# Optimization experiments

Measured on AMD Instinct MI355X. Metric: run time of the kernel, lower is better.

The kernel has to match this reference:

```python
import jax, jax.numpy as jnp
import numpy as np
from jax import lax

SPARSITY = 0.5  # args.sparsity: fraction of weights KEPT


def get_subnet(scores, k):
    """GetSubnet.forward: sort |scores|, zero lowest (1-k) fraction, one elsewhere."""
    sa = jnp.abs(scores)
    n = sa.size
    j = int((1.0 - k) * n)  # static: number of entries zeroed
    idx = jnp.argsort(sa.ravel())  # ascending, matches torch .sort()
    mask = jnp.zeros((n,), dtype=sa.dtype).at[idx[j:]].set(1.0)
    return mask.reshape(scores.shape)


def masked_conv(x, w, s, b, stride):
    m = get_subnet(s, SPARSITY)
    y = lax.conv_general_dilated(
        x, w * m, window_strides=(stride, stride), padding=((1, 1), (1, 1)),
        dimension_numbers=('NCHW', 'OIHW', 'NCHW'))
    return y + b[None, :, None, None]


def setup_inputs() -> dict:
    key = jax.random.key(0)
    ks = jax.random.split(key, 16)
    def rn(k, shape, scale):
        return jax.random.normal(k, shape, dtype=jnp.float32) * scale
    return {
        'x':   rn(ks[0], (64, 3, 64, 64), 1.0),
        'w1':  rn(ks[1], (128, 3, 3, 3), 0.2),   's1': rn(ks[2], (128, 3, 3, 3), 1.0),   'b1': rn(ks[3], (128,), 0.01),
        'w2':  rn(ks[4], (256, 128, 3, 3), 0.05), 's2': rn(ks[5], (256, 128, 3, 3), 1.0), 'b2': rn(ks[6], (256,), 0.01),
        'w3':  rn(ks[7], (512, 256, 3, 3), 0.03), 's3': rn(ks[8], (512, 256, 3, 3), 1.0), 'b3': rn(ks[9], (512,), 0.01),
        'fw1': rn(ks[10], (1024, 512), 0.05),     'fs1': rn(ks[11], (1024, 512), 1.0),    'fb1': rn(ks[12], (1024,), 0.01),
        'fw2': rn(ks[13], (10, 1024), 0.05),      'fs2': rn(ks[14], (10, 1024), 1.0),     'fb2': rn(ks[15], (10,), 0.01),
    }


def reference(x, w1, s1, b1, w2, s2, b2, w3, s3, b3, fw1, fs1, fb1, fw2, fs2, fb2):
    h = jax.nn.relu(masked_conv(x, w1, s1, b1, stride=1))   # [64,128,64,64]
    h = jax.nn.relu(masked_conv(h, w2, s2, b2, stride=2))   # [64,256,32,32]
    h = jax.nn.relu(masked_conv(h, w3, s3, b3, stride=2))   # [64,512,16,16]
    h = h.mean(axis=(2, 3))                                 # [64,512] global avg pool
    m1 = get_subnet(fs1, SPARSITY)
    h = jax.nn.relu(h @ (fw1 * m1).T + fb1)                 # [64,1024]
    m2 = get_subnet(fs2, SPARSITY)
    return h @ (fw2 * m2).T + fb2                           # [64,10]
```

## Files before the change

### kernel.cpp

```cpp
#include <hip/hip_runtime.h>
#include <stdint.h>


typedef __attribute__((ext_vector_type(8))) short short8;
typedef __attribute__((ext_vector_type(4))) short short4v;
typedef __attribute__((ext_vector_type(4))) float floatx4;

__device__ __forceinline__ unsigned short f2bf(float f) {
    unsigned u = __float_as_uint(f);
    u += 0x7fffu + ((u >> 16) & 1u);
    return (unsigned short)(u >> 16);
}

constexpr unsigned CUM0 = 3456u;
constexpr unsigned CUM1 = 298368u;
constexpr unsigned CUM2 = 1478016u;
constexpr unsigned CUM3 = 2002304u;
constexpr unsigned STOT = 2012544u;
constexpr int NBH = 512;

__device__ __forceinline__ int find_tensor(unsigned idx, unsigned& li) {
    if (idx < CUM0) { li = idx;        return 0; }
    if (idx < CUM1) { li = idx - CUM0; return 1; }
    if (idx < CUM2) { li = idx - CUM1; return 2; }
    if (idx < CUM3) { li = idx - CUM2; return 3; }
    li = idx - CUM3; return 4;
}

__global__ __launch_bounds__(256) void hist11(const float* __restrict__ s0,
                                              const float* __restrict__ s1,
                                              const float* __restrict__ s2,
                                              const float* __restrict__ s3,
                                              const float* __restrict__ s4,
                                              const unsigned* __restrict__ P,
                                              unsigned* __restrict__ ghist, int pass) {
    __shared__ unsigned lh[10240];
    const int tid = threadIdx.x;
    const int NB = (pass == 2) ? 512 : 2048;
    for (int i = tid; i < NB * 5; i += 256) lh[i] = 0;
    __syncthreads();

    unsigned pref[5];
    #pragma unroll
    for (int t = 0; t < 5; t++) pref[t] = pass ? P[t] : 0u;
    const int fsh = (pass == 1) ? 20 : 9;

    for (unsigned idx = blockIdx.x * 256u + tid; idx < STOT; idx += NBH * 256u) {
        unsigned li; int t = find_tensor(idx, li);
        const float* sp = t == 0 ? s0 : t == 1 ? s1 : t == 2 ? s2 : t == 3 ? s3 : s4;
        unsigned key = __float_as_uint(sp[li]) & 0x7fffffffu;
        bool ok = (pass == 0) || ((key >> fsh) == pref[t]);
        if (ok) {
            unsigned bin = (pass == 0) ? (key >> 20)
                         : (pass == 1) ? ((key >> 9) & 2047u)
                                       : (key & 511u);
            atomicAdd(&lh[(unsigned)t * NB + bin], 1u);
        }
    }
    __syncthreads();
    const int goff = (pass == 0) ? 0 : (pass == 1) ? 10240 : 20480;
    for (int i = tid; i < NB * 5; i += 256) {
        unsigned v = lh[i];
        if (v) atomicAdd(&ghist[goff + i], v);
    }
}

__global__ __launch_bounds__(256) void find11(const unsigned* __restrict__ ghist,
                                              unsigned* __restrict__ P,
                                              unsigned* __restrict__ targ, int pass) {
    const int t = blockIdx.x;
    const int tid = threadIdx.x;
    const int NB = (pass == 2) ? 512 : 2048;
    const int goff = (pass == 0) ? 0 : (pass == 1) ? 10240 : 20480;
    const int seg = NB / 256;
    __shared__ unsigned bins[2048];
    __shared__ unsigned part[256];
    for (int i = tid; i < NB; i += 256) bins[i] = ghist[goff + t * NB + i];
    __syncthreads();
    unsigned s = 0;
    for (int j = 0; j < seg; j++) s += bins[tid * seg + j];
    part[tid] = s;
    __syncthreads();
    if (tid == 0) {
        unsigned n = t == 0 ? 3456u : t == 1 ? 294912u : t == 2 ? 1179648u
                   : t == 3 ? 524288u : 10240u;
        unsigned target = (pass == 0) ? (n >> 1) : targ[t];
        unsigned cum = 0; int q = 0;
        for (; q < 256; q++) { unsigned c = part[q]; if (cum + c > target) break; cum += c; }
        int b = q * seg;
        for (;; b++) { unsigned c = bins[b]; if (cum + c > target) break; cum += c; }
        targ[t] = target - cum;
        if (pass == 0)      P[t] = (unsigned)b;
        else if (pass == 1) P[t] = (P[t] << 11) | (unsigned)b;
        else                P[t] = (P[t] << 9) | (unsigned)b;
    }
}

__global__ void mask_reorder(const float* __restrict__ w0, const float* __restrict__ w1,
                             const float* __restrict__ w2, const float* __restrict__ w3,
                             const float* __restrict__ w4,
                             const float* __restrict__ s0, const float* __restrict__ s1,
                             const float* __restrict__ s2, const float* __restrict__ s3,
                             const float* __restrict__ s4,
                             const unsigned* __restrict__ T,
                             float* __restrict__ wm1,
                             unsigned short* __restrict__ A2,
                             unsigned short* __restrict__ A3,
                             float* __restrict__ fwm1, float* __restrict__ fwm2,
                             float* __restrict__ pooled) {
    unsigned idx = blockIdx.x * 256u + threadIdx.x;
    if (idx >= STOT) return;
    if (idx < 32768u) pooled[idx] = 0.f;
    unsigned li; int t = find_tensor(idx, li);
    const float* sp = t == 0 ? s0 : t == 1 ? s1 : t == 2 ? s2 : t == 3 ? s3 : s4;
    const float* wp = t == 0 ? w0 : t == 1 ? w1 : t == 2 ? w2 : t == 3 ? w3 : w4;
    unsigned key = __float_as_uint(sp[li]) & 0x7fffffffu;
    float val = (key >= T[t]) ? wp[li] : 0.f;
    if (t == 0) {
        wm1[li] = val;
    } else if (t == 1) {
        unsigned k = li / 1152u, r = li - k * 1152u;
        unsigned c = r / 9u, e = r - c * 9u;
        A2[((size_t)e * 256u + k) * 128u + c] = f2bf(val);
    } else if (t == 2) {
        unsigned k = li / 2304u, r = li - k * 2304u;
        unsigned c = r / 9u, e = r - c * 9u;
        A3[((size_t)e * 512u + k) * 256u + c] = f2bf(val);
    } else if (t == 3) {
        fwm1[li] = val;
    } else {
        fwm2[li] = val;
    }
}

template <int C, int H, int W, int K, int TX, int TY, int KT>
__global__ __launch_bounds__(TX* TY) void conv_direct(const float* __restrict__ in,
                                                      const float* __restrict__ wm,
                                                      const float* __restrict__ bias,
                                                      unsigned short* __restrict__ out) {
    constexpr int TILW = TX * 2, TILH = TY * 2;
    constexpr int ITW = TILW + 2, ITH = TILH + 2;
    constexpr int NTHREADS = TX * TY;
    constexpr int NLOAD = (ITH * ITW + NTHREADS - 1) / NTHREADS;
    constexpr int KG = K / KT;

    __shared__ float sIn[ITH * ITW];
    __shared__ float sW[9 * KT];

    const int tid = threadIdx.x;
    const int tx = tid % TX, ty = tid / TX;
    const int kg = blockIdx.z % KG, n = blockIdx.z / KG;
    const int ox0 = blockIdx.x * TILW, oy0 = blockIdx.y * TILH;
    const int ix0 = ox0 - 1, iy0 = oy0 - 1;

    const float* inN = in + (size_t)n * C * H * W;
    const float* wkg = wm + (size_t)kg * KT * C * 9;

    int goff[NLOAD];
    #pragma unroll
    for (int i = 0; i < NLOAD; i++) {
        int idx = tid + i * NTHREADS;
        if (idx < ITH * ITW) {
            int r = idx / ITW, col = idx % ITW;
            int gy = iy0 + r, gx = ix0 + col;
            goff[i] = (gy >= 0 && gy < H && gx >= 0 && gx < W) ? (gy * W + gx) : -1;
        } else goff[i] = -2;
    }

    float acc[2][2][KT];
    #pragma unroll
    for (int py = 0; py < 2; py++)
        #pragma unroll
        for (int px = 0; px < 2; px++)
            #pragma unroll
            for (int j = 0; j < KT; j++) acc[py][px][j] = 0.f;

    for (int c = 0; c < C; c++) {
        const float* inC = inN + (size_t)c * H * W;
        #pragma unroll
        for (int i = 0; i < NLOAD; i++) {
            int g = goff[i];
            if (g >= -1) sIn[tid + i * NTHREADS] = (g >= 0) ? inC[g] : 0.f;
        }
        for (int i = tid; i < 9 * KT; i += NTHREADS) {
            int e = i / KT, j = i % KT;
            sW[i] = wkg[j * C * 9 + c * 9 + e];
        }
        __syncthreads();

        float vin[4][4];
        const float* base = &sIn[(ty * 2) * ITW + tx * 2];
        #pragma unroll
        for (int r = 0; r < 4; r++)
            #pragma unroll
            for (int cc = 0; cc < 4; cc++) vin[r][cc] = base[r * ITW + cc];

        #pragma unroll
        for (int e = 0; e < 9; e++) {
            const int dy = e / 3, dx = e % 3;
            #pragma unroll
            for (int j = 0; j < KT; j++) {
                float wv = sW[e * KT + j];
                #pragma unroll
                for (int py = 0; py < 2; py++)
                    #pragma unroll
                    for (int px = 0; px < 2; px++)
                        acc[py][px][j] = fmaf(vin[py + dy][px + dx], wv, acc[py][px][j]);
            }
        }
        __syncthreads();
    }

    float bj[KT];
    #pragma unroll
    for (int j = 0; j < KT; j++) bj[j] = bias[kg * KT + j];
    #pragma unroll
    for (int py = 0; py < 2; py++)
        #pragma unroll
        for (int px = 0; px < 2; px++) {
            int oy = oy0 + ty * 2 + py, ox = ox0 + tx * 2 + px;
            short8 v;
            #pragma unroll
            for (int j = 0; j < KT; j++) {
                float t = acc[py][px][j] + bj[j];
                v[j] = (short)f2bf(t > 0.f ? t : 0.f);
            }
            *(short8*)(out + ((size_t)(n * H + oy) * W + ox) * K + kg * KT) = v;
        }
}

template <int C, int H, int W, int KOUT, int NPIX, bool POOL, bool SWAPYZ>
__global__ __launch_bounds__(256, 4) void conv_mfma(const unsigned short* __restrict__ in,
                                                    const unsigned short* __restrict__ A,
                                                    const float* __restrict__ bias,
                                                    void* __restrict__ outv) {
    constexpr int OH = H / 2, OW = W / 2;
    constexpr int PR = NPIX / OW;
    constexpr int FN = NPIX / 16;
    constexpr int RH = 2 * PR + 1;
    constexpr int IW = W + 1;
    constexpr int NC = C / 32;
    constexpr int PSTR = 40;
    constexpr int NSLOT = RH * IW * 4;
    constexpr int SLMAX = (NSLOT + 255) / 256;

    __shared__ unsigned short sIn[RH * IW * PSTR];

    const int tid = threadIdx.x;
    const int lane = tid & 63;
    const int wv = tid >> 6;
    const int l15 = lane & 15;
    const int quad = lane >> 4;
    const int pt = blockIdx.x;
    const int kb = SWAPYZ ? blockIdx.z : blockIdx.y;
    const int n  = SWAPYZ ? blockIdx.y : blockIdx.z;
    const int k0 = kb * 128;
    const int oy0 = pt * PR;
    const int g0y = 2 * oy0 - 1;
    const int mw = wv * 32;

    int goff[SLMAX], slds[SLMAX];
    #pragma unroll
    for (int i = 0; i < SLMAX; i++) {
        int s = tid + i * 256;
        if (s < NSLOT) {
            int q = s & 3, pix = s >> 2;
            int ix = pix % IW, iy = pix / IW;
            int gy = g0y + iy, gx = ix - 1;
            slds[i] = pix * PSTR + q * 8;
            goff[i] = (gy >= 0 && gy < H && gx >= 0) ? ((gy * W + gx) * C + q * 8) : -1;
        } else { goff[i] = -2; slds[i] = 0; }
    }

    int pB[FN];
    #pragma unroll
    for (int fn = 0; fn < FN; fn++) {
        int p = fn * 16 + l15;
        int oyl = p / OW, oxl = p % OW;
        pB[fn] = (oyl * 2 * IW + oxl * 2) * PSTR + quad * 8;
    }

    const unsigned short* inN = in + (size_t)n * H * W * C;

    floatx4 acc[2][FN];
    #pragma unroll
    for (int fm = 0; fm < 2; fm++)
        #pragma unroll
        for (int fn = 0; fn < FN; fn++) acc[fm][fn] = (floatx4){0.f, 0.f, 0.f, 0.f};

    short8 st[SLMAX];
    #pragma unroll
    for (int i = 0; i < SLMAX; i++) {
        int g = goff[i];
        if (g >= 0) st[i] = *(const short8*)(inN + g);
    }

    for (int cc = 0; cc < NC; cc++) {
        const int cof = cc * 32;
        #pragma unroll
        for (int i = 0; i < SLMAX; i++) {
            int g = goff[i];
            if (g >= 0) {
                *(short8*)&sIn[slds[i]] = st[i];
            } else if (g == -1 && cc == 0) {
                *(short8*)&sIn[slds[i]] = (short8){0, 0, 0, 0, 0, 0, 0, 0};
            }
        }
        __syncthreads();
        if (cc + 1 < NC) {
            const int ncof = cof + 32;
            #pragma unroll
            for (int i = 0; i < SLMAX; i++) {
                int g = goff[i];
                if (g >= 0) st[i] = *(const short8*)(inN + g + ncof);
            }
        }

        const unsigned short* Abase = A + (size_t)(k0 + mw + l15) * C + cof + quad * 8;
        const size_t estr = (size_t)KOUT * C;

        short8 a0 = *(const short8*)(Abase);
        short8 a1 = *(const short8*)(Abase + 16 * C);

        #pragma unroll 1
        for (int e = 0; e < 9; e++) {
            short8 ac0 = a0, ac1 = a1;
            if (e < 8) {
                a0 = *(const short8*)(Abase + (size_t)(e + 1) * estr);
                a1 = *(const short8*)(Abase + (size_t)(e + 1) * estr + 16 * C);
            }
            const int dy = e / 3, dx = e - dy * 3;
            const int boff = (dy * IW + dx) * PSTR;
            short8 bfr[FN];
            #pragma unroll
            for (int fn = 0; fn < FN; fn++)
                bfr[fn] = *(const short8*)&sIn[pB[fn] + boff];
            #pragma unroll
            for (int fn = 0; fn < FN; fn++) {
                acc[0][fn] = __builtin_amdgcn_mfma_f32_16x16x32_bf16(ac0, bfr[fn], acc[0][fn], 0, 0, 0);
                acc[1][fn] = __builtin_amdgcn_mfma_f32_16x16x32_bf16(ac1, bfr[fn], acc[1][fn], 0, 0, 0);
            }
        }
        __syncthreads();
    }

    if (!POOL) {
        unsigned short* out = (unsigned short*)outv;
        #pragma unroll
        for (int fm = 0; fm < 2; fm++) {
            const int k4 = k0 + mw + fm * 16 + quad * 4;
            float b0 = bias[k4], b1 = bias[k4 + 1], b2 = bias[k4 + 2], b3 = bias[k4 + 3];
            #pragma unroll
            for (int fn = 0; fn < FN; fn++) {
                int p = fn * 16 + l15;
                int oy = oy0 + p / OW, ox = p % OW;
                float v0 = acc[fm][fn][0] + b0, v1 = acc[fm][fn][1] + b1;
                float v2 = acc[fm][fn][2] + b2, v3 = acc[fm][fn][3] + b3;
                short4v v;
                v[0] = (short)f2bf(v0 > 0.f ? v0 : 0.f);
                v[1] = (short)f2bf(v1 > 0.f ? v1 : 0.f);
                v[2] = (short)f2bf(v2 > 0.f ? v2 : 0.f);
                v[3] = (short)f2bf(v3 > 0.f ? v3 : 0.f);
                *(short4v*)(out + ((size_t)(n * OH + oy) * OW + ox) * KOUT + k4) = v;
            }
        }
    } else {
        float* out = (float*)outv;
        #pragma unroll
        for (int fm = 0; fm < 2; fm++) {
            #pragma unroll
            for (int reg = 0; reg < 4; reg++) {
                int k = k0 + mw + fm * 16 + quad * 4 + reg;
                float bv = bias[k];
                float s = 0.f;
                #pragma unroll
                for (int fn = 0; fn < FN; fn++) {
                    float v = acc[fm][fn][reg] + bv;
                    s += v > 0.f ? v : 0.f;
                }
                s += __shfl_xor(s, 1); s += __shfl_xor(s, 2);
                s += __shfl_xor(s, 4); s += __shfl_xor(s, 8);
                if (l15 == 0) atomicAdd(&out[n * KOUT + k], s * (1.0f / (OH * OW)));
            }
        }
    }
}

__global__ void fc1_kernel(const float* __restrict__ pooled, const float* __restrict__ w,
                           const float* __restrict__ b, float* __restrict__ out) {
    int t = blockIdx.x * 256 + threadIdx.x;
    int o = t & 1023, n = t >> 10;
    const float4* w4 = (const float4*)(w + (size_t)o * 512);
    const float4* p4 = (const float4*)(pooled + (size_t)n * 512);
    float acc = 0.f;
    for (int i = 0; i < 128; i++) {
        float4 a = p4[i], ww = w4[i];
        acc += a.x * ww.x + a.y * ww.y + a.z * ww.z + a.w * ww.w;
    }
    acc += b[o];
    out[t] = acc > 0.f ? acc : 0.f;
}

__global__ void fc2_kernel(const float* __restrict__ h, const float* __restrict__ w,
                           const float* __restrict__ b, float* __restrict__ out) {
    int n = blockIdx.x, tid = threadIdx.x;
    __shared__ float redw[40];
    const float4* h4 = (const float4*)(h + (size_t)n * 1024);
    float4 a = h4[tid];
    for (int o = 0; o < 10; o++) {
        const float4* w4 = (const float4*)(w + (size_t)o * 1024);
        float4 ww = w4[tid];
        float v = a.x * ww.x + a.y * ww.y + a.z * ww.z + a.w * ww.w;
        for (int off = 32; off > 0; off >>= 1) v += __shfl_down(v, off);
        if ((tid & 63) == 0) redw[o * 4 + (tid >> 6)] = v;
    }
    __syncthreads();
    if (tid < 10) {
        float s = redw[tid * 4] + redw[tid * 4 + 1] + redw[tid * 4 + 2] + redw[tid * 4 + 3] + b[tid];
        out[n * 10 + tid] = s;
    }
}

extern "C" void kernel_launch(void* const* d_in, const int* in_sizes, int n_in,
                              void* d_out, int out_size, void* d_ws, size_t ws_size,
                              hipStream_t stream) {
    const float* x   = (const float*)d_in[0];
    const float* w1  = (const float*)d_in[1];
    const float* s1  = (const float*)d_in[2];
    const float* b1  = (const float*)d_in[3];
    const float* w2  = (const float*)d_in[4];
    const float* s2  = (const float*)d_in[5];
    const float* b2  = (const float*)d_in[6];
    const float* w3  = (const float*)d_in[7];
    const float* s3  = (const float*)d_in[8];
    const float* b3  = (const float*)d_in[9];
    const float* fw1 = (const float*)d_in[10];
    const float* fs1 = (const float*)d_in[11];
    const float* fb1 = (const float*)d_in[12];
    const float* fw2 = (const float*)d_in[13];
    const float* fs2 = (const float*)d_in[14];
    const float* fb2 = (const float*)d_in[15];
    float* out = (float*)d_out;

    char* ws = (char*)d_ws;
    size_t off = 0;
    auto alloc = [&](size_t bytes) -> char* {
        char* p = ws + off;
        off = (off + bytes + 255) & ~(size_t)255;
        return p;
    };
    unsigned* ghist = (unsigned*)alloc(23040ull * 4);
    unsigned* P     = (unsigned*)alloc(64);
    unsigned* targ  = (unsigned*)alloc(64);
    float* wm1  = (float*)alloc(3456ull * 4);
    float* fwm1 = (float*)alloc(524288ull * 4);
    float* fwm2 = (float*)alloc(10240ull * 4);
    unsigned short* A2 = (unsigned short*)alloc(294912ull * 2);
    unsigned short* A3 = (unsigned short*)alloc(1179648ull * 2);
    unsigned short* h1 = (unsigned short*)alloc(33554432ull * 2);
    unsigned short* h2 = (unsigned short*)alloc(16777216ull * 2);
    float* pooled = (float*)alloc(32768ull * 4);
    float* fc1h   = (float*)alloc(65536ull * 4);
    if (off > ws_size) return;

    (void)hipMemsetAsync(ghist, 0, 23040ull * 4, stream);

    for (int pass = 0; pass < 3; pass++) {
        hist11<<<NBH, 256, 0, stream>>>(s1, s2, s3, fs1, fs2, P, ghist, pass);
        find11<<<5, 256, 0, stream>>>(ghist, P, targ, pass);
    }
    int gs = (STOT + 255) / 256;
    mask_reorder<<<gs, 256, 0, stream>>>(w1, w2, w3, fw1, fw2, s1, s2, s3, fs1, fs2, P,
                                         wm1, A2, A3, fwm1, fwm2, pooled);

    conv_direct<3, 64, 64, 128, 16, 16, 8>
        <<<dim3(2, 2, 64 * 16), 256, 0, stream>>>(x, wm1, b1, h1);
    conv_mfma<128, 64, 64, 256, 64, false, false>
        <<<dim3(16, 2, 64), 256, 0, stream>>>(h1, A2, b2, h2);
    conv_mfma<256, 32, 32, 512, 64, true, true>
        <<<dim3(4, 64, 4), 256, 0, stream>>>(h2, A3, b3, pooled);

    fc1_kernel<<<256, 256, 0, stream>>>(pooled, fwm1, fb1, fc1h);
    fc2_kernel<<<64, 256, 0, stream>>>(fc1h, fwm2, fb2, out);
}
```

Before: 424.2 us.

## Unroll tap loop with deeper A/B fragment prefetch, drop cross-chunk register staging

Drops the register-staged prefetch of the next input channel chunk, which overlapped global loads with compute across chunks. Global input is now loaded straight into LDS each chunk. In its place the 9-tap loop is fully unrolled: weight fragments are prefetched two taps ahead and LDS fragments one tap ahead, so MFMAs can overlap loads within a chunk. This trades the cross-chunk overlap for intra-chunk scheduling and raises register pressure, which may cut occupancy.

Measured after the change: 420.0 us. No clear change (-1.0%).

```diff
diff --git a/kernel.cpp b/kernel.cpp
--- a/kernel.cpp
+++ b/kernel.cpp
@@ -288,60 +288,56 @@
         #pragma unroll
         for (int fn = 0; fn < FN; fn++) acc[fm][fn] = (floatx4){0.f, 0.f, 0.f, 0.f};
 
-    short8 st[SLMAX];
-    #pragma unroll
-    for (int i = 0; i < SLMAX; i++) {
-        int g = goff[i];
-        if (g >= 0) st[i] = *(const short8*)(inN + g);
-    }
-
+    #pragma unroll 1
     for (int cc = 0; cc < NC; cc++) {
         const int cof = cc * 32;
+        const unsigned short* Abase = A + (size_t)(k0 + mw + l15) * C + cof + quad * 8;
+        const size_t estr = (size_t)KOUT * C;
+
+        __syncthreads();
+
+        short8 af[9][2];
+        short8 bf[9][FN];
+
+        af[0][0] = *(const short8*)(Abase);
+        af[0][1] = *(const short8*)(Abase + 16 * C);
+        af[1][0] = *(const short8*)(Abase + estr);
+        af[1][1] = *(const short8*)(Abase + estr + 16 * C);
+
         #pragma unroll
         for (int i = 0; i < SLMAX; i++) {
             int g = goff[i];
             if (g >= 0) {
-                *(short8*)&sIn[slds[i]] = st[i];
+                *(short8*)&sIn[slds[i]] = *(const short8*)(inN + g + cof);
             } else if (g == -1 && cc == 0) {
                 *(short8*)&sIn[slds[i]] = (short8){0, 0, 0, 0, 0, 0, 0, 0};
             }
         }
         __syncthreads();
-        if (cc + 1 < NC) {
-            const int ncof = cof + 32;
-            #pragma unroll
-            for (int i = 0; i < SLMAX; i++) {
-                int g = goff[i];
-                if (g >= 0) st[i] = *(const short8*)(inN + g + ncof);
-            }
-        }
-
-        const unsigned short* Abase = A + (size_t)(k0 + mw + l15) * C + cof + quad * 8;
-        const size_t estr = (size_t)KOUT * C;
-
-        short8 a0 = *(const short8*)(Abase);
-        short8 a1 = *(const short8*)(Abase + 16 * C);
-
-        #pragma unroll 1
+
+        #pragma unroll
+        for (int fn = 0; fn < FN; fn++)
+            bf[0][fn] = *(const short8*)&sIn[pB[fn]];
+
+        #pragma unroll
         for (int e = 0; e < 9; e++) {
-            short8 ac0 = a0, ac1 = a1;
-            if (e < 8) {
-                a0 = *(const short8*)(Abase + (size_t)(e + 1) * estr);
-                a1 = *(const short8*)(Abase + (size_t)(e + 1) * estr + 16 * C);
-            }
-            const int dy = e / 3, dx = e - dy * 3;
-            const int boff = (dy * IW + dx) * PSTR;
-            short8 bfr[FN];
-            #pragma unroll
-            for (int fn = 0; fn < FN; fn++)
-                bfr[fn] = *(const short8*)&sIn[pB[fn] + boff];
+            if (e + 2 < 9) {
+                af[e + 2][0] = *(const short8*)(Abase + (size_t)(e + 2) * estr);
+                af[e + 2][1] = *(const short8*)(Abase + (size_t)(e + 2) * estr + 16 * C);
+            }
+            if (e + 1 < 9) {
+                const int dy1 = (e + 1) / 3, dx1 = (e + 1) - dy1 * 3;
+                const int boff = (dy1 * IW + dx1) * PSTR;
+                #pragma unroll
+                for (int fn = 0; fn < FN; fn++)
+                    bf[e + 1][fn] = *(const short8*)&sIn[pB[fn] + boff];
+            }
             #pragma unroll
             for (int fn = 0; fn < FN; fn++) {
-                acc[0][fn] = __builtin_amdgcn_mfma_f32_16x16x32_bf16(ac0, bfr[fn], acc[0][fn], 0, 0, 0);
-                acc[1][fn] = __builtin_amdgcn_mfma_f32_16x16x32_bf16(ac1, bfr[fn], acc[1][fn], 0, 0, 0);
-            }
-        }
-        __syncthreads();
+                acc[0][fn] = __builtin_amdgcn_mfma_f32_16x16x32_bf16(af[e][0], bf[e][fn], acc[0][fn], 0, 0, 0);
+                acc[1][fn] = __builtin_amdgcn_mfma_f32_16x16x32_bf16(af[e][1], bf[e][fn], acc[1][fn], 0, 0, 0);
+            }
+        }
     }
 
     if (!POOL) {
```
